# Kernel tuning notes

Hardware: AMD Instinct MI355X
Metric: run time of the kernel (lower is better)

Reference implementation:

```python
import jax, jax.numpy as jnp
import numpy as np

NUM_HEADS = 16
D_MODEL = 1024
D_K = D_MODEL // NUM_HEADS


def setup_inputs() -> dict:
    key = jax.random.key(0)
    ks = jax.random.split(key, 11)
    B, S, D = 1, 4096, D_MODEL
    scale = 1.0 / np.sqrt(D)
    return {
        "Q": jax.random.normal(ks[0], (B, S, D), jnp.float32),
        "K": jax.random.normal(ks[1], (B, S, D), jnp.float32),
        "V": jax.random.normal(ks[2], (B, S, D), jnp.float32),
        "W_Q": jax.random.normal(ks[3], (D, D), jnp.float32) * scale,
        "b_Q": jax.random.normal(ks[4], (D,), jnp.float32) * 0.02,
        "W_K": jax.random.normal(ks[5], (D, D), jnp.float32) * scale,
        "b_K": jax.random.normal(ks[6], (D,), jnp.float32) * 0.02,
        "W_V": jax.random.normal(ks[7], (D, D), jnp.float32) * scale,
        "b_V": jax.random.normal(ks[8], (D,), jnp.float32) * 0.02,
        "W_O": jax.random.normal(ks[9], (D, D), jnp.float32) * scale,
        "b_O": jax.random.normal(ks[10], (D,), jnp.float32) * 0.02,
    }


def _split_heads(x):
    # (B, S, D) -> (B, H, S, d_k)
    B, S, _ = x.shape
    return x.reshape(B, S, NUM_HEADS, D_K).transpose(0, 2, 1, 3)


def reference(Q, K, V, W_Q, b_Q, W_K, b_K, W_V, b_V, W_O, b_O):
    q = _split_heads(Q @ W_Q + b_Q)  # (B, H, S, d_k)
    k = _split_heads(K @ W_K + b_K)
    v = _split_heads(V @ W_V + b_V)
    inv_sqrt_dk = jnp.asarray(1.0 / np.sqrt(D_K), q.dtype)
    scores = jnp.einsum("bhqd,bhkd->bhqk", q, k) * inv_sqrt_dk  # (B, H, S, S)
    weights = jax.nn.softmax(scores, axis=-1)
    out = jnp.einsum("bhqk,bhkd->bhqd", weights, v)  # (B, H, S, d_k)
    B, _, S, _ = out.shape
    combined = out.transpose(0, 2, 1, 3).reshape(B, S, D_MODEL)
    return combined @ W_O + b_O
```

## Files before the change

kernel.cpp:

```cpp
#include <hip/hip_runtime.h>

typedef float f32x2 __attribute__((ext_vector_type(2)));
typedef float f32x4 __attribute__((ext_vector_type(4)));
typedef float f32x16 __attribute__((ext_vector_type(16)));
typedef short bf16x8 __attribute__((ext_vector_type(8)));
typedef unsigned u32x2 __attribute__((ext_vector_type(2)));
typedef unsigned short u16;

#define S_LEN 4096
#define DMODEL 1024
#define NH 16
#define DK 64

#define SCALE_Q 0.18033688f

static __device__ __forceinline__ u16 f2bf(float x) {
  union { float f; unsigned u; } v; v.f = x;
  unsigned r = v.u + 0x7fffu + ((v.u >> 16) & 1u);
  return (u16)(r >> 16);
}

static __device__ __forceinline__ float bf2f(u16 x) {
  union { unsigned u; float f; } v; v.u = ((unsigned)x) << 16;
  return v.f;
}

#if __has_builtin(__builtin_amdgcn_exp2f)
#define EXP2F __builtin_amdgcn_exp2f
#else
#define EXP2F exp2f
#endif

static __device__ __forceinline__ unsigned pkbf(float lo, float hi) {
  unsigned r;
  asm("v_cvt_pk_bf16_f32 %0, %1, %2" : "=v"(r) : "v"(lo), "v"(hi));
  return r;
}

static __device__ __forceinline__ void plswap(unsigned& a, unsigned& b, int hi) {
#if __has_builtin(__builtin_amdgcn_permlane32_swap)
  u32x2 r = __builtin_amdgcn_permlane32_swap(a, b, false, false);
  a = r.x; b = r.y;
  (void)hi;
#else
  unsigned ax = __shfl_xor(a, 32), bx = __shfl_xor(b, 32);
  unsigned na = hi ? bx : a;
  unsigned nb = hi ? b : ax;
  a = na; b = nb;
#endif
}

static __device__ __forceinline__ void gload16(const void* g, void* l) {
  void* gg = (void*)g;
  __builtin_amdgcn_global_load_lds(
      (__attribute__((address_space(1))) void*)gg,
      (__attribute__((address_space(3))) void*)l, 16, 0, 0);
}

__global__ __launch_bounds__(256) void prep(const float* __restrict__ W0,
                                            const float* __restrict__ W1,
                                            const float* __restrict__ W2,
                                            const float* __restrict__ W3,
                                            u16* __restrict__ Wt,
                                            const float* __restrict__ Q,
                                            const float* __restrict__ K,
                                            const float* __restrict__ V,
                                            u16* __restrict__ Qbf) {
  __shared__ float t[32][33];
  const int b = blockIdx.x;
  const int tid = threadIdx.x;
  if (b < 4096) {
    const int z = b >> 10;
    const int rem = b & 1023;
    const float* W = (z == 0) ? W0 : (z == 1) ? W1 : (z == 2) ? W2 : W3;
    u16* dst = Wt + (size_t)z * DMODEL * DMODEL;
    const int x = tid & 31, y = tid >> 5;
    const int n0 = (rem & 31) * 32, k0 = (rem >> 5) * 32;
#pragma unroll
    for (int i = 0; i < 4; ++i)
      t[y + 8 * i][x] = W[(size_t)(k0 + y + 8 * i) * DMODEL + n0 + x];
    __syncthreads();
#pragma unroll
    for (int i = 0; i < 4; ++i)
      dst[(size_t)(n0 + y + 8 * i) * DMODEL + k0 + x] = f2bf(t[x][y + 8 * i]);
  } else {
    const int b2 = b - 4096;
    const int z = b2 >> 10;
    const int blk = b2 & 1023;
    const float* src = (z == 0) ? Q : (z == 1) ? K : V;
    u16* dst = Qbf + (size_t)z * S_LEN * DMODEL;
    const int n8 = S_LEN * DMODEL / 8;
    for (int i = blk * 256 + tid; i < n8; i += 1024 * 256) {
      float4 a = ((const float4*)src)[2 * i];
      float4 c = ((const float4*)src)[2 * i + 1];
      union { ushort4 u[2]; int4 q; } tt;
      tt.u[0].x = f2bf(a.x); tt.u[0].y = f2bf(a.y);
      tt.u[0].z = f2bf(a.z); tt.u[0].w = f2bf(a.w);
      tt.u[1].x = f2bf(c.x); tt.u[1].y = f2bf(c.y);
      tt.u[1].z = f2bf(c.z); tt.u[1].w = f2bf(c.w);
      ((int4*)dst)[i] = tt.q;
    }
  }
}

__global__ __launch_bounds__(256) void pgemm(const u16* __restrict__ Abase,
                                             const u16* __restrict__ Btbase,
                                             const float* __restrict__ bq,
                                             const float* __restrict__ bk,
                                             const float* __restrict__ bv,
                                             void* __restrict__ outbase) {
  __shared__ __align__(16) char smem[65536];
  const int nblk = gridDim.x, cpx = nblk >> 3;
  const int b0 = blockIdx.x;
  const int bid = (b0 & 7) * cpx + (b0 >> 3);
  const int z = bid >> 8;
  const int rem = bid & 255;
  const int nb = rem & 7, mb = rem >> 3;
  const int m0 = mb * 128, n0 = nb * 128;
  const int tid = threadIdx.x, lane = tid & 63, wid = tid >> 6;
  const int l31 = lane & 31, hi = lane >> 5;
  const int wm = (wid >> 1) * 64, wn = (wid & 1) * 64;
  const char* Ab = (const char*)(Abase + (size_t)z * S_LEN * DMODEL);
  const char* Bb = (const char*)(Btbase + (size_t)z * DMODEL * DMODEL);
  const float* bias = (z == 0) ? bq : (z == 1 ? bk : bv);
  const float scale = (z == 0) ? SCALE_Q : 1.0f;

  f32x16 acc[2][2] = {};

  float bb2[2];
#pragma unroll
  for (int g = 0; g < 2; ++g) bb2[g] = bias[n0 + wn + g * 32 + l31];
  asm volatile("s_waitcnt vmcnt(0)" ::: "memory");

  const int r8 = tid >> 3;
  const int colg = ((tid * 16) & 127) ^ ((r8 & 7) << 4);
  const char* gA = Ab + (size_t)(m0 + r8) * 2048 + colg;
  const char* gB = Bb + (size_t)(n0 + r8) * 2048 + colg;
  const int ldst = wid * 1024;

  auto stageAB = [&](int base) {
#pragma unroll
    for (int p = 0; p < 4; ++p)
      gload16(gA + p * 65536, smem + base + p * 4096 + ldst);
#pragma unroll
    for (int p = 0; p < 4; ++p)
      gload16(gB + p * 65536, smem + base + 16384 + p * 4096 + ldst);
    gA += 128; gB += 128;
  };

  auto compute = [&](int base) {
    const char* Al = smem + base;
    const char* Bl = smem + base + 16384;
#pragma unroll
    for (int ks = 0; ks < 4; ++ks) {
      bf16x8 a2[2], b2[2];
#pragma unroll
      for (int f = 0; f < 2; ++f) {
        int row = wm + f * 32 + l31;
        a2[f] = *(const bf16x8*)(Al + row * 128 +
                                 ((ks * 32 + hi * 16) ^ ((row & 7) << 4)));
      }
#pragma unroll
      for (int g = 0; g < 2; ++g) {
        int row = wn + g * 32 + l31;
        b2[g] = *(const bf16x8*)(Bl + row * 128 +
                                 ((ks * 32 + hi * 16) ^ ((row & 7) << 4)));
      }
#pragma unroll
      for (int f = 0; f < 2; ++f)
#pragma unroll
        for (int g = 0; g < 2; ++g)
          acc[f][g] =
              __builtin_amdgcn_mfma_f32_32x32x16_bf16(a2[f], b2[g], acc[f][g], 0, 0, 0);
    }
  };

  auto body = [&](const int CUR, const int NXT, bool doStage) {
    __builtin_amdgcn_sched_barrier(0);
    if (doStage) {
      stageAB(NXT);
      asm volatile("s_waitcnt vmcnt(8)" ::: "memory");
    } else {
      asm volatile("s_waitcnt vmcnt(0)" ::: "memory");
    }
    __builtin_amdgcn_s_barrier();
    compute(CUR);
    __builtin_amdgcn_s_barrier();
  };

  stageAB(0);
  for (int kt = 0; kt < 16; kt += 2) {
    body(0, 32768, kt + 1 < 16);
    body(32768, 0, kt + 2 < 16);
  }

#pragma unroll
  for (int f = 0; f < 2; ++f) {
#pragma unroll
    for (int g = 0; g < 2; ++g) {
      const int col = n0 + wn + g * 32 + l31;
      const int row0 = m0 + wm + f * 32 + 4 * hi;
      const float bb = bb2[g];
      if (z == 2) {
        u16* ov = (u16*)outbase + (size_t)2 * S_LEN * DMODEL;
        u16* base = ov + ((size_t)(col >> 6) * DK + (col & 63)) * S_LEN;
#pragma unroll
        for (int q2 = 0; q2 < 4; ++q2) {
          const int row = row0 + 8 * q2;
          ushort4 u;
          u.x = f2bf(acc[f][g][4 * q2 + 0] + bb);
          u.y = f2bf(acc[f][g][4 * q2 + 1] + bb);
          u.z = f2bf(acc[f][g][4 * q2 + 2] + bb);
          u.w = f2bf(acc[f][g][4 * q2 + 3] + bb);
          *(ushort4*)(base + row) = u;
        }
      } else {
        u16* oq = (u16*)outbase + (size_t)z * S_LEN * DMODEL;
#pragma unroll
        for (int i = 0; i < 16; ++i) {
          const int row = row0 + (i & 3) + 8 * (i >> 2);
          oq[((size_t)(col >> 6) * S_LEN + row) * DK + (col & 63)] =
              f2bf((acc[f][g][i] + bb) * scale);
        }
      }
    }
  }
}

__global__ __launch_bounds__(256) void ogemm(const u16* __restrict__ A,
                                             const u16* __restrict__ Bt,
                                             const float* __restrict__ bias,
                                             float* __restrict__ out) {
  __shared__ __align__(16) char smem[49152];
  const int b0 = blockIdx.x;
  const int bid = (b0 & 7) * 64 + (b0 >> 3);
  const int nb = bid & 7, mb = bid >> 3;
  const int m0 = mb * 64, n0 = nb * 128;
  const int tid = threadIdx.x, lane = tid & 63, wid = tid >> 6;
  const int l31 = lane & 31, hi = lane >> 5;
  const int wm = (wid >> 1) * 32, wn = (wid & 1) * 64;

  f32x16 acc[2] = {};

  float bb2[2];
#pragma unroll
  for (int g = 0; g < 2; ++g) bb2[g] = bias[n0 + wn + g * 32 + l31];
  asm volatile("s_waitcnt vmcnt(0)" ::: "memory");

  const int r8 = tid >> 3;
  const int colg = ((tid * 16) & 127) ^ ((r8 & 7) << 4);
  const char* gA = (const char*)A + (size_t)(m0 + r8) * 2048 + colg;
  const char* gB = (const char*)Bt + (size_t)(n0 + r8) * 2048 + colg;
  const int ldst = wid * 1024;

  auto stageAB = [&](int base) {
#pragma unroll
    for (int p = 0; p < 2; ++p)
      gload16(gA + p * 65536, smem + base + p * 4096 + ldst);
#pragma unroll
    for (int p = 0; p < 4; ++p)
      gload16(gB + p * 65536, smem + base + 8192 + p * 4096 + ldst);
    gA += 128; gB += 128;
  };

  auto compute = [&](int base) {
    const char* Al = smem + base;
    const char* Bl = smem + base + 8192;
#pragma unroll
    for (int ks = 0; ks < 4; ++ks) {
      int rowA = wm + l31;
      bf16x8 a2 = *(const bf16x8*)(Al + rowA * 128 +
                                   ((ks * 32 + hi * 16) ^ ((rowA & 7) << 4)));
      bf16x8 b2[2];
#pragma unroll
      for (int g = 0; g < 2; ++g) {
        int row = wn + g * 32 + l31;
        b2[g] = *(const bf16x8*)(Bl + row * 128 +
                                 ((ks * 32 + hi * 16) ^ ((row & 7) << 4)));
      }
#pragma unroll
      for (int g = 0; g < 2; ++g)
        acc[g] = __builtin_amdgcn_mfma_f32_32x32x16_bf16(a2, b2[g], acc[g], 0, 0, 0);
    }
  };

  auto body = [&](const int CUR, const int NXT, bool doStage) {
    __builtin_amdgcn_sched_barrier(0);
    if (doStage) {
      stageAB(NXT);
      asm volatile("s_waitcnt vmcnt(6)" ::: "memory");
    } else {
      asm volatile("s_waitcnt vmcnt(0)" ::: "memory");
    }
    __builtin_amdgcn_s_barrier();
    compute(CUR);
    __builtin_amdgcn_s_barrier();
  };

  stageAB(0);
  for (int kt = 0; kt < 16; kt += 2) {
    body(0, 24576, kt + 1 < 16);
    body(24576, 0, kt + 2 < 16);
  }

#pragma unroll
  for (int g = 0; g < 2; ++g) {
    const int col = n0 + wn + g * 32 + l31;
    const int row0 = m0 + wm + 4 * hi;
    const float bb = bb2[g];
#pragma unroll
    for (int i = 0; i < 16; ++i) {
      const int row = row0 + (i & 3) + 8 * (i >> 2);
      out[(size_t)row * DMODEL + col] = acc[g][i] + bb;
    }
  }
}

__global__ __launch_bounds__(512) void attn2(const u16* __restrict__ q,
                                             const u16* __restrict__ k,
                                             const u16* __restrict__ vt,
                                             u16* __restrict__ Opart,
                                             float* __restrict__ Lpart) {
  __shared__ __align__(16) char smem[32768];
  const int bid0 = blockIdx.x;
  const int bid = (bid0 & 7) * 64 + (bid0 >> 3);
  const int h = bid >> 5;
  const int kvh = (bid >> 4) & 1;
  const int qblk = bid & 15;
  const int tid = threadIdx.x;
  const int wid = tid >> 6, lane = tid & 63;
  const int l31 = lane & 31, hi = lane >> 5;

  const char* kpb = (const char*)k + (size_t)h * S_LEN * (DK * 2);
  const char* vtb = (const char*)vt + (size_t)h * DK * (S_LEN * 2);

  const int q0w = qblk * 256 + wid * 32;
  const u16* qrow = q + ((size_t)h * S_LEN + q0w + l31) * DK;
  bf16x8 qf[4];
#pragma unroll
  for (int dt = 0; dt < 4; ++dt)
    qf[dt] = *(const bf16x8*)(qrow + dt * 16 + hi * 8);

  f32x16 o0 = {}, o1 = {};
  f32x2 lacc2 = {0.f, 0.f};

  const int woff = wid << 10;
  const int kt0 = kvh * 32;
  const int kt1 = kt0 + 32;

  const int swz = (l31 & 7) << 4;
  int dsa[4];
#pragma unroll
  for (int dt = 0; dt < 4; ++dt)
    dsa[dt] = (l31 << 7) + ((dt * 32 + hi * 16) ^ swz);

  const int lin = tid * 16;
  const int sw = lin ^ (((lin >> 7) & 7) << 4);
  const char* gk = kpb + (size_t)kt0 * 8192 + sw;
  const char* gv = vtb + (size_t)(lin >> 7) * 8192 + (size_t)kt0 * 128 + (sw & 127);

  gload16(gk, smem + woff);          gk += 8192;
  gload16(gv, smem + 8192 + woff);   gv += 128;

  auto body = [&](const int CUR, const int NXT, bool doStage) {
    if (doStage) {
      gload16(gk, smem + NXT + woff);          gk += 8192;
      gload16(gv, smem + NXT + 8192 + woff);   gv += 128;
      asm volatile("s_waitcnt vmcnt(2)" ::: "memory");
    } else {
      asm volatile("s_waitcnt vmcnt(0)" ::: "memory");
    }
    __builtin_amdgcn_s_barrier();

    const char* kb = smem + CUR;
    const char* vb = smem + CUR + 8192;

    f32x16 st0 = {}, st1 = {};
    __builtin_amdgcn_s_setprio(1);
#pragma unroll
    for (int dt = 0; dt < 4; ++dt) {
      bf16x8 k0 = *(const bf16x8*)(kb + dsa[dt]);
      bf16x8 k1 = *(const bf16x8*)(kb + 4096 + dsa[dt]);
      st0 = __builtin_amdgcn_mfma_f32_32x32x16_bf16(k0, qf[dt], st0, 0, 0, 0);
      st1 = __builtin_amdgcn_mfma_f32_32x32x16_bf16(k1, qf[dt], st1, 0, 0, 0);
    }
    __builtin_amdgcn_s_setprio(0);

    unsigned w0[8], w1[8];
    f32x2 s2 = {0.f, 0.f};
#pragma unroll
    for (int i = 0; i < 8; ++i) {
      float a0 = EXP2F(st0[2 * i]), a1 = EXP2F(st0[2 * i + 1]);
      f32x2 t = {a0, a1}; s2 += t;
      w0[i] = pkbf(a0, a1);
    }
#pragma unroll
    for (int i = 0; i < 8; ++i) {
      float a0 = EXP2F(st1[2 * i]), a1 = EXP2F(st1[2 * i + 1]);
      f32x2 t = {a0, a1}; s2 += t;
      w1[i] = pkbf(a0, a1);
    }
    lacc2 += s2;

    union UF { unsigned w[4]; bf16x8 v; };
    UF f[4];
#pragma unroll
    for (int g = 0; g < 2; ++g) {
#pragma unroll
      for (int j = 0; j < 2; ++j) {
        unsigned a = w0[4 * g + j], b = w0[4 * g + j + 2];
        plswap(a, b, hi);
        f[g].w[j] = a; f[g].w[j + 2] = b;
        unsigned c = w1[4 * g + j], d = w1[4 * g + j + 2];
        plswap(c, d, hi);
        f[2 + g].w[j] = c; f[2 + g].w[j + 2] = d;
      }
    }

    __builtin_amdgcn_s_setprio(1);
#pragma unroll
    for (int kt2 = 0; kt2 < 4; ++kt2) {
      bf16x8 v0 = *(const bf16x8*)(vb + dsa[kt2]);
      bf16x8 v1 = *(const bf16x8*)(vb + 4096 + dsa[kt2]);
      o0 = __builtin_amdgcn_mfma_f32_32x32x16_bf16(v0, f[kt2].v, o0, 0, 0, 0);
      o1 = __builtin_amdgcn_mfma_f32_32x32x16_bf16(v1, f[kt2].v, o1, 0, 0, 0);
    }
    __builtin_amdgcn_s_setprio(0);

    __builtin_amdgcn_s_barrier();
  };

  for (int kt = kt0; kt < kt1; kt += 2) {
    body(0, 16384, kt + 1 < kt1);
    body(16384, 0, kt + 2 < kt1);
  }

  const float lacc = lacc2.x + lacc2.y;
  const float lrow = lacc + __shfl_xor(lacc, 32);
  u16* Ob = Opart + ((((size_t)kvh * NH + h) * S_LEN) + q0w + l31) * DK;
#pragma unroll
  for (int g = 0; g < 4; ++g) {
    ushort4 u0, u1;
    u0.x = f2bf(o0[g * 4 + 0]); u0.y = f2bf(o0[g * 4 + 1]);
    u0.z = f2bf(o0[g * 4 + 2]); u0.w = f2bf(o0[g * 4 + 3]);
    *(ushort4*)(Ob + 8 * g + 4 * hi) = u0;
    u1.x = f2bf(o1[g * 4 + 0]); u1.y = f2bf(o1[g * 4 + 1]);
    u1.z = f2bf(o1[g * 4 + 2]); u1.w = f2bf(o1[g * 4 + 3]);
    *(ushort4*)(Ob + 32 + 8 * g + 4 * hi) = u1;
  }
  Lpart[((size_t)kvh * NH + h) * S_LEN + q0w + l31] = lrow;
}

__global__ __launch_bounds__(256) void combine(const u16* __restrict__ Op,
                                               const float* __restrict__ Lp,
                                               u16* __restrict__ comb) {
  const int id = blockIdx.x * 256 + threadIdx.x;
  const int h = id >> 16;
  const int rem = id & 65535;
  const int qv = rem >> 4;
  const int d4 = (rem & 15) << 2;
  const size_t str = (size_t)NH * S_LEN * DK;
  const size_t base = (((size_t)h * S_LEN) + qv) * DK + d4;
  float o0 = 0.f, o1 = 0.f, o2 = 0.f, o3 = 0.f, l = 0.f;
#pragma unroll
  for (int kv = 0; kv < 2; ++kv) {
    ushort4 u = *(const ushort4*)(Op + kv * str + base);
    o0 += bf2f(u.x); o1 += bf2f(u.y); o2 += bf2f(u.z); o3 += bf2f(u.w);
    l += Lp[(size_t)kv * NH * S_LEN + (size_t)h * S_LEN + qv];
  }
  const float inv = 1.f / l;
  ushort4 u;
  u.x = f2bf(o0 * inv);
  u.y = f2bf(o1 * inv);
  u.z = f2bf(o2 * inv);
  u.w = f2bf(o3 * inv);
  *(ushort4*)(comb + (size_t)qv * DMODEL + h * DK + d4) = u;
}

extern "C" void kernel_launch(void* const* d_in, const int* in_sizes, int n_in,
                              void* d_out, int out_size, void* d_ws, size_t ws_size,
                              hipStream_t stream) {
  (void)in_sizes; (void)n_in; (void)out_size; (void)ws_size;
  const float* Q   = (const float*)d_in[0];
  const float* K   = (const float*)d_in[1];
  const float* V   = (const float*)d_in[2];
  const float* W_Q = (const float*)d_in[3];
  const float* b_Q = (const float*)d_in[4];
  const float* W_K = (const float*)d_in[5];
  const float* b_K = (const float*)d_in[6];
  const float* W_V = (const float*)d_in[7];
  const float* b_V = (const float*)d_in[8];
  const float* W_O = (const float*)d_in[9];
  const float* b_O = (const float*)d_in[10];
  float* out = (float*)d_out;

  char* ws = (char*)d_ws;
  const size_t MB = 1024 * 1024;
  u16* WtQ = (u16*)ws;
  u16* Qbf = (u16*)(ws + 8 * MB);
  u16* Opart = (u16*)(ws + 8 * MB);
  u16* qp   = (u16*)(ws + 40 * MB);
  u16* kp   = qp + (size_t)S_LEN * DMODEL;
  u16* vtp  = kp + (size_t)S_LEN * DMODEL;
  u16* comb = vtp + (size_t)S_LEN * DMODEL;
  float* Lpart = (float*)(ws + 72 * MB);

  prep<<<7168, 256, 0, stream>>>(W_Q, W_K, W_V, W_O, WtQ, Q, K, V, Qbf);

  pgemm<<<768, 256, 0, stream>>>(Qbf, WtQ, b_Q, b_K, b_V, qp);

  attn2<<<512, 512, 0, stream>>>(qp, kp, vtp, Opart, Lpart);
  combine<<<4096, 256, 0, stream>>>(Opart, Lpart, comb);

  ogemm<<<512, 256, 0, stream>>>(comb, WtQ + (size_t)3 * DMODEL * DMODEL,
                                 b_O, out);
}
```

Before: 154.8 us.

## Fuse split-KV combine into output projection GEMM A-tile staging

Removes the separate combine kernel and instead sums the two partial attention outputs and normalizes by the summed row sums while staging the A tile of the output-projection GEMM. This eliminates a kernel launch and the write/read round-trip of the combined bf16 activation buffer. In exchange the A tile is loaded through registers with synchronous global loads and LDS stores rather than direct async global-to-LDS loads, which may expose latency in the pipelined loop.

```diff
diff --git a/kernel.cpp b/kernel.cpp
--- a/kernel.cpp
+++ b/kernel.cpp
@@ -22,6 +22,11 @@
 
 static __device__ __forceinline__ float bf2f(u16 x) {
   union { unsigned u; float f; } v; v.u = ((unsigned)x) << 16;
+  return v.f;
+}
+
+static __device__ __forceinline__ float asf(unsigned u) {
+  union { unsigned u; float f; } v; v.u = u;
   return v.f;
 }
 
@@ -227,10 +232,11 @@
   }
 }
 
-__global__ __launch_bounds__(256) void ogemm(const u16* __restrict__ A,
-                                             const u16* __restrict__ Bt,
-                                             const float* __restrict__ bias,
-                                             float* __restrict__ out) {
+__global__ __launch_bounds__(256) void ogemm2(const u16* __restrict__ Op,
+                                              const float* __restrict__ Lp,
+                                              const u16* __restrict__ Bt,
+                                              const float* __restrict__ bias,
+                                              float* __restrict__ out) {
   __shared__ __align__(16) char smem[49152];
   const int b0 = blockIdx.x;
   const int bid = (b0 & 7) * 64 + (b0 >> 3);
@@ -239,6 +245,7 @@
   const int tid = threadIdx.x, lane = tid & 63, wid = tid >> 6;
   const int l31 = lane & 31, hi = lane >> 5;
   const int wm = (wid >> 1) * 32, wn = (wid & 1) * 64;
+  const size_t halfO = (size_t)NH * S_LEN * DK;
 
   f32x16 acc[2] = {};
 
@@ -248,19 +255,49 @@
   asm volatile("s_waitcnt vmcnt(0)" ::: "memory");
 
   const int r8 = tid >> 3;
-  const int colg = ((tid * 16) & 127) ^ ((r8 & 7) << 4);
-  const char* gA = (const char*)A + (size_t)(m0 + r8) * 2048 + colg;
-  const char* gB = (const char*)Bt + (size_t)(n0 + r8) * 2048 + colg;
-  const int ldst = wid * 1024;
-
-  auto stageAB = [&](int base) {
-#pragma unroll
-    for (int p = 0; p < 2; ++p)
-      gload16(gA + p * 65536, smem + base + p * 4096 + ldst);
+  const int c8 = tid & 7;
+  const int colgB = ((tid * 16) & 127) ^ ((r8 & 7) << 4);
+  const char* gB = (const char*)Bt + (size_t)(n0 + r8) * 2048 + colgB;
+  const int ldstB = wid * 1024;
+
+  auto stageB = [&](int base) {
 #pragma unroll
     for (int p = 0; p < 4; ++p)
-      gload16(gB + p * 65536, smem + base + 8192 + p * 4096 + ldst);
-    gA += 128; gB += 128;
+      gload16(gB + p * 65536, smem + base + 8192 + p * 4096 + ldstB);
+    gB += 128;
+  };
+
+  auto loadA = [&](int kt, int4& a0, int4& b0, int4& a1, int4& b1,
+                   float& inv0, float& inv1) {
+    const size_t base0 = ((size_t)kt * S_LEN + m0 + r8) * DK + c8 * 8;
+    const size_t base1 = base0 + (size_t)32 * DK;
+    a0 = *(const int4*)(Op + base0);
+    b0 = *(const int4*)(Op + halfO + base0);
+    a1 = *(const int4*)(Op + base1);
+    b1 = *(const int4*)(Op + halfO + base1);
+    const size_t lb0 = (size_t)kt * S_LEN + m0 + r8;
+    inv0 = 1.f / (Lp[lb0] + Lp[(size_t)NH * S_LEN + lb0]);
+    inv1 = 1.f / (Lp[lb0 + 32] + Lp[(size_t)NH * S_LEN + lb0 + 32]);
+  };
+
+  auto writeA = [&](int base, int4 a, int4 b, float inv, int row) {
+    unsigned w[4];
+#pragma unroll
+    for (int j = 0; j < 4; ++j) {
+      unsigned ua = ((unsigned*)&a)[j], ub = ((unsigned*)&b)[j];
+      float lo = asf(ua << 16) + asf(ub << 16);
+      float hh = asf(ua & 0xffff0000u) + asf(ub & 0xffff0000u);
+      w[j] = pkbf(lo * inv, hh * inv);
+    }
+    const int addr = base + row * 128 + ((c8 * 16) ^ ((row & 7) << 4));
+    *(int4*)(smem + addr) = *(int4*)w;
+  };
+
+  auto stageA = [&](int base, int kt) {
+    int4 a0, b0, a1, b1; float i0, i1;
+    loadA(kt, a0, b0, a1, b1, i0, i1);
+    writeA(base, a0, b0, i0, r8);
+    writeA(base, a1, b1, i1, 32 + r8);
   };
 
   auto compute = [&](int base) {
@@ -284,23 +321,30 @@
     }
   };
 
-  auto body = [&](const int CUR, const int NXT, bool doStage) {
+  auto body = [&](const int CUR, const int NXT, int ktn, bool doStage) {
     __builtin_amdgcn_sched_barrier(0);
     if (doStage) {
-      stageAB(NXT);
-      asm volatile("s_waitcnt vmcnt(6)" ::: "memory");
+      int4 a0, b0, a1, b1; float i0, i1;
+      loadA(ktn, a0, b0, a1, b1, i0, i1);
+      stageB(NXT);
+      writeA(NXT, a0, b0, i0, r8);
+      writeA(NXT, a1, b1, i1, 32 + r8);
+      asm volatile("s_waitcnt vmcnt(4) lgkmcnt(0)" ::: "memory");
     } else {
-      asm volatile("s_waitcnt vmcnt(0)" ::: "memory");
+      asm volatile("s_waitcnt vmcnt(0) lgkmcnt(0)" ::: "memory");
     }
     __builtin_amdgcn_s_barrier();
     compute(CUR);
     __builtin_amdgcn_s_barrier();
   };
 
-  stageAB(0);
+  stageB(0);
+  stageA(0, 0);
+  asm volatile("s_waitcnt lgkmcnt(0)" ::: "memory");
+
   for (int kt = 0; kt < 16; kt += 2) {
-    body(0, 24576, kt + 1 < 16);
-    body(24576, 0, kt + 2 < 16);
+    body(0, 24576, kt + 1, kt + 1 < 16);
+    body(24576, 0, kt + 2, kt + 2 < 16);
   }
 
 #pragma unroll
@@ -449,32 +493,6 @@
     *(ushort4*)(Ob + 32 + 8 * g + 4 * hi) = u1;
   }
   Lpart[((size_t)kvh * NH + h) * S_LEN + q0w + l31] = lrow;
-}
-
-__global__ __launch_bounds__(256) void combine(const u16* __restrict__ Op,
-                                               const float* __restrict__ Lp,
-                                               u16* __restrict__ comb) {
-  const int id = blockIdx.x * 256 + threadIdx.x;
-  const int h = id >> 16;
-  const int rem = id & 65535;
-  const int qv = rem >> 4;
-  const int d4 = (rem & 15) << 2;
-  const size_t str = (size_t)NH * S_LEN * DK;
-  const size_t base = (((size_t)h * S_LEN) + qv) * DK + d4;
-  float o0 = 0.f, o1 = 0.f, o2 = 0.f, o3 = 0.f, l = 0.f;
-#pragma unroll
-  for (int kv = 0; kv < 2; ++kv) {
-    ushort4 u = *(const ushort4*)(Op + kv * str + base);
-    o0 += bf2f(u.x); o1 += bf2f(u.y); o2 += bf2f(u.z); o3 += bf2f(u.w);
-    l += Lp[(size_t)kv * NH * S_LEN + (size_t)h * S_LEN + qv];
-  }
-  const float inv = 1.f / l;
-  ushort4 u;
-  u.x = f2bf(o0 * inv);
-  u.y = f2bf(o1 * inv);
-  u.z = f2bf(o2 * inv);
-  u.w = f2bf(o3 * inv);
-  *(ushort4*)(comb + (size_t)qv * DMODEL + h * DK + d4) = u;
 }
 
 extern "C" void kernel_launch(void* const* d_in, const int* in_sizes, int n_in,
@@ -502,7 +520,6 @@
   u16* qp   = (u16*)(ws + 40 * MB);
   u16* kp   = qp + (size_t)S_LEN * DMODEL;
   u16* vtp  = kp + (size_t)S_LEN * DMODEL;
-  u16* comb = vtp + (size_t)S_LEN * DMODEL;
   float* Lpart = (float*)(ws + 72 * MB);
 
   prep<<<7168, 256, 0, stream>>>(W_Q, W_K, W_V, W_O, WtQ, Q, K, V, Qbf);
@@ -510,8 +527,7 @@
   pgemm<<<768, 256, 0, stream>>>(Qbf, WtQ, b_Q, b_K, b_V, qp);
 
   attn2<<<512, 512, 0, stream>>>(qp, kp, vtp, Opart, Lpart);
-  combine<<<4096, 256, 0, stream>>>(Opart, Lpart, comb);
-
-  ogemm<<<512, 256, 0, stream>>>(comb, WtQ + (size_t)3 * DMODEL * DMODEL,
-                                 b_O, out);
-}
+
+  ogemm2<<<512, 256, 0, stream>>>(Opart, Lpart,
+                                  WtQ + (size_t)3 * DMODEL * DMODEL, b_O, out);
+}
```

Result: slower. 158.3 us (+2.3%).
